# Kernel tuning notes

Hardware: AMD Instinct MI355X
Metric: run time of the kernel (lower is better)

Reference implementation:

```python
import jax, jax.numpy as jnp
import numpy as np

B, MQ, MK = 8, 512, 2048
Q_DIM, KV_DIM = 1024, 256
H = 8
QKC, VC = 1024, 1024
DQ, DV = QKC // H, VC // H
EPS = 1e-5  # nn.LayerNorm default


def _layer_norm(x, w, b):
    m = jnp.mean(x, axis=-1, keepdims=True)
    v = jnp.var(x, axis=-1, keepdims=True)
    return (x - m) * jax.lax.rsqrt(v + EPS) * w + b


def setup_inputs() -> dict:
    key = jax.random.key(0)
    ks = jax.random.split(key, 12)
    hidden_states = jax.random.normal(ks[0], (B, MQ, Q_DIM), dtype=jnp.float32)
    inputs = jax.random.normal(ks[1], (B, MK, KV_DIM), dtype=jnp.float32)
    # ragged per-batch kv lengths -> prefix-valid mask (matches keys[i, :n] packing)
    lengths = jax.random.randint(ks[2], (B,), MK // 4, MK + 1)
    inputs_mask = (jnp.arange(MK)[None, :] < lengths[:, None]).astype(jnp.int32)
    s = 0.02
    return {
        "hidden_states": hidden_states,
        "inputs": inputs,
        "inputs_mask": inputs_mask,
        "ln1_w": jnp.ones((Q_DIM,), jnp.float32),
        "ln1_b": jnp.zeros((Q_DIM,), jnp.float32),
        "ln2_w": jnp.ones((KV_DIM,), jnp.float32),
        "ln2_b": jnp.zeros((KV_DIM,), jnp.float32),
        "Wq": s * jax.random.normal(ks[3], (Q_DIM, QKC), dtype=jnp.float32),
        "bq": jnp.zeros((QKC,), jnp.float32),
        "Wk": s * jax.random.normal(ks[4], (KV_DIM, QKC), dtype=jnp.float32),
        "bk": jnp.zeros((QKC,), jnp.float32),
        "Wv": s * jax.random.normal(ks[5], (KV_DIM, VC), dtype=jnp.float32),
        "bv": jnp.zeros((VC,), jnp.float32),
    }


def reference(hidden_states, inputs, inputs_mask, ln1_w, ln1_b, ln2_w, ln2_b,
              Wq, bq, Wk, bk, Wv, bv):
    hs = _layer_norm(hidden_states, ln1_w, ln1_b)      # [B, MQ, Q_DIM]
    kv = _layer_norm(inputs, ln2_w, ln2_b)             # [B, MK, KV_DIM]

    q = (hs @ Wq + bq).reshape(B, MQ, H, DQ)           # [B, MQ, H, DQ]
    k = (kv @ Wk + bk).reshape(B, MK, H, DQ)           # [B, MK, H, DQ]
    v = (kv @ Wv + bv).reshape(B, MK, H, DV)           # [B, MK, H, DV]

    scores = jnp.einsum("bqhd,bkhd->bhqk", q, k) / jnp.sqrt(jnp.float32(DQ))
    mask_f = inputs_mask.astype(scores.dtype)          # [B, MK]
    neg = jnp.finfo(scores.dtype).min
    scores = scores + (1.0 - mask_f)[:, None, None, :] * neg
    probs = jax.nn.softmax(scores, axis=-1)            # [B, H, MQ, MK]

    ctx = jnp.einsum("bhqk,bkhd->bqhd", probs, v)      # [B, MQ, H, DV]
    return ctx.reshape(B, MQ, H * DV)
```

## Files before the change

### kernel.cpp

```cpp
#include <hip/hip_runtime.h>

#define DI __device__ __forceinline__

typedef _Float16 f16x8 __attribute__((ext_vector_type(8)));
typedef _Float16 f16x4 __attribute__((ext_vector_type(4)));
typedef float    f32x4 __attribute__((ext_vector_type(4)));

namespace {

constexpr int kB  = 8;
constexpr int kMQ = 512;
constexpr int kMK = 2048;
constexpr int kQKC = 1024;
constexpr int kVC  = 1024;

DI void gload16(const void* g, void* l) {
  __builtin_amdgcn_global_load_lds(
      (const __attribute__((address_space(1))) void*)g,
      (__attribute__((address_space(3))) void*)l, 16, 0, 0);
}

DI f32x4 mfma16(f16x8 a, f16x8 b, f32x4 c) {
  return __builtin_amdgcn_mfma_f32_16x16x32_f16(a, b, c, 0, 0, 0);
}

DI f32x4 mfma16k16(f16x4 a, f16x4 b, f32x4 c) {
  return __builtin_amdgcn_mfma_f32_16x16x16f16(a, b, c, 0, 0, 0);
}

template<int K, int N>
DI void transpose_dev(const float* __restrict__ W, _Float16* __restrict__ WT,
                      int bid, float (*t)[65]) {
  int nt = bid % (N / 64), kt = bid / (N / 64);
  int k0 = kt * 64, n0 = nt * 64;
  int tid = threadIdx.x;
#pragma unroll
  for (int j = 0; j < 16; ++j) {
    int e = tid + j * 256;
    int r = e >> 6, c = e & 63;
    t[r][c] = W[(size_t)(k0 + r) * N + n0 + c];
  }
  __syncthreads();
#pragma unroll
  for (int j = 0; j < 16; ++j) {
    int e = tid + j * 256;
    int r = e >> 6, c = e & 63;
    WT[(size_t)(n0 + r) * K + k0 + c] = (_Float16)t[c][r];
  }
}

DI void ln1024_dev(const float* __restrict__ x, const float* __restrict__ w,
                   const float* __restrict__ bb, _Float16* __restrict__ y,
                   int row, float* red) {
  int tid = threadIdx.x;
  const float4* xr = (const float4*)(x + (size_t)row * 1024);
  float4 v = xr[tid];
  float s = v.x + v.y + v.z + v.w;
  float q = v.x * v.x + v.y * v.y + v.z * v.z + v.w * v.w;
#pragma unroll
  for (int m = 32; m; m >>= 1) { s += __shfl_xor(s, m); q += __shfl_xor(q, m); }
  if ((tid & 63) == 0) { red[tid >> 6] = s; red[4 + (tid >> 6)] = q; }
  __syncthreads();
  s = red[0] + red[1] + red[2] + red[3];
  q = red[4] + red[5] + red[6] + red[7];
  float mean = s * (1.0f / 1024.0f);
  float var = q * (1.0f / 1024.0f) - mean * mean;
  float inv = rsqrtf(var + 1e-5f);
  f16x4 o;
  const float* wp = w + tid * 4;
  const float* bp = bb + tid * 4;
  o[0] = (_Float16)((v.x - mean) * inv * wp[0] + bp[0]);
  o[1] = (_Float16)((v.y - mean) * inv * wp[1] + bp[1]);
  o[2] = (_Float16)((v.z - mean) * inv * wp[2] + bp[2]);
  o[3] = (_Float16)((v.w - mean) * inv * wp[3] + bp[3]);
  *(f16x4*)(y + (size_t)row * 1024 + tid * 4) = o;
}

DI void ln256_dev(const float* __restrict__ x, const float* __restrict__ w,
                  const float* __restrict__ bb, _Float16* __restrict__ y, int bid) {
  int tid = threadIdx.x;
  int lane = tid & 63, wv = tid >> 6;
  size_t row = (size_t)bid * 4 + wv;
  const float4* xr = (const float4*)(x + row * 256);
  float4 v = xr[lane];
  float s = v.x + v.y + v.z + v.w;
  float q = v.x * v.x + v.y * v.y + v.z * v.z + v.w * v.w;
#pragma unroll
  for (int m = 32; m; m >>= 1) { s += __shfl_xor(s, m); q += __shfl_xor(q, m); }
  float mean = s * (1.0f / 256.0f);
  float var = q * (1.0f / 256.0f) - mean * mean;
  float inv = rsqrtf(var + 1e-5f);
  f16x4 o;
  const float* wp = w + lane * 4;
  const float* bp = bb + lane * 4;
  o[0] = (_Float16)((v.x - mean) * inv * wp[0] + bp[0]);
  o[1] = (_Float16)((v.y - mean) * inv * wp[1] + bp[1]);
  o[2] = (_Float16)((v.z - mean) * inv * wp[2] + bp[2]);
  o[3] = (_Float16)((v.w - mean) * inv * wp[3] + bp[3]);
  *(f16x4*)(y + row * 256 + lane * 4) = o;
}

__global__ __launch_bounds__(256) void prep_all(
    const float* __restrict__ Wq, const float* __restrict__ Wk, const float* __restrict__ Wv,
    _Float16* __restrict__ WqT, _Float16* __restrict__ WkT, _Float16* __restrict__ WvT,
    const float* __restrict__ hs, const float* __restrict__ ln1w, const float* __restrict__ ln1b,
    _Float16* __restrict__ hsln,
    const float* __restrict__ xin, const float* __restrict__ ln2w, const float* __restrict__ ln2b,
    _Float16* __restrict__ kvln) {
  __shared__ float tbuf[64][65];
  int bid = blockIdx.x;
  if (bid < 256) {
    transpose_dev<1024, 1024>(Wq, WqT, bid, tbuf);
  } else if (bid < 320) {
    transpose_dev<256, 1024>(Wk, WkT, bid - 256, tbuf);
  } else if (bid < 384) {
    transpose_dev<256, 1024>(Wv, WvT, bid - 320, tbuf);
  } else if (bid < 4480) {
    ln1024_dev(hs, ln1w, ln1b, hsln, bid - 384, (float*)tbuf);
  } else {
    ln256_dev(xin, ln2w, ln2b, kvln, bid - 4480);
  }
}

template<int M, int N, int K, bool BIAS_ROW, int MMODE, bool CM>
DI void gemm_dev(const _Float16* __restrict__ A, const _Float16* __restrict__ Bt,
                 const float* __restrict__ bias, const int* __restrict__ msk,
                 _Float16* __restrict__ C, int bid,
                 _Float16 (*As)[128 * 64], _Float16 (*Bs)[128 * 64]) {
  int tid = threadIdx.x, lane = tid & 63;
  int w = tid >> 6, wr = w >> 1, wc = w & 1;
  constexpr int NT = N / 128;
  constexpr int MT = M / 128;
  constexpr int KT = K / 64;
  int mt, nt;
  if constexpr (CM) { mt = bid % MT; nt = bid / MT; }
  else              { mt = bid / NT; nt = bid % NT; }
  if constexpr (MMODE == 1) { if (msk[mt * 128] == 0) return; }
  if constexpr (MMODE == 2) { if (msk[nt * 128] == 0) return; }
  const int l15 = lane & 15, l4 = lane >> 4;

  f32x4 acc[4][4] = {};

  const int rS = tid >> 3;
  const int cpS = tid & 7;

  auto stage = [&](int kt, int bufi) {
#pragma unroll
    for (int j = 0; j < 4; ++j) {
      int rr = rS + j * 32;
      int cg = cpS ^ (rr & 7);
      gload16(A  + ((size_t)(mt * 128 + rr) * K + kt * 64 + cg * 8),
              (char*)As[bufi] + j * 4096 + tid * 16);
      gload16(Bt + ((size_t)(nt * 128 + rr) * K + kt * 64 + cg * 8),
              (char*)Bs[bufi] + j * 4096 + tid * 16);
    }
  };

  stage(0, 0);
  __syncthreads();

  for (int kt = 0; kt < KT; ++kt) {
    int cur = kt & 1;
    if (kt + 1 < KT) stage(kt + 1, cur ^ 1);
#pragma unroll
    for (int ss = 0; ss < 2; ++ss) {
      f16x8 a[4], b[4];
#pragma unroll
      for (int m = 0; m < 4; ++m) {
        int ra = wr * 64 + m * 16 + l15;
        int cl = ss * 4 + l4;
        a[m] = *(const f16x8*)((const char*)As[cur] + ra * 128 + ((cl ^ (ra & 7)) << 4));
        int rb = wc * 64 + m * 16 + l15;
        b[m] = *(const f16x8*)((const char*)Bs[cur] + rb * 128 + ((cl ^ (rb & 7)) << 4));
      }
#pragma unroll
      for (int m = 0; m < 4; ++m)
#pragma unroll
        for (int n = 0; n < 4; ++n)
          acc[m][n] = mfma16(a[m], b[n], acc[m][n]);
    }
    __syncthreads();
  }

#pragma unroll
  for (int m = 0; m < 4; ++m) {
#pragma unroll
    for (int n = 0; n < 4; ++n) {
      int gi0 = mt * 128 + wr * 64 + m * 16 + l4 * 4;
      int gj  = nt * 128 + wc * 64 + n * 16 + l15;
#pragma unroll
      for (int r = 0; r < 4; ++r) {
        int gi = gi0 + r;
        float v = acc[m][n][r] + (BIAS_ROW ? bias[gi] : bias[gj]);
        C[(size_t)gi * N + gj] = (_Float16)v;
      }
    }
  }
}

__global__ __launch_bounds__(256) void gemm_all(
    const _Float16* __restrict__ hsln, const _Float16* __restrict__ WqT,
    const float* __restrict__ bq, _Float16* __restrict__ qbf,
    const _Float16* __restrict__ kvln, const _Float16* __restrict__ WkT,
    const float* __restrict__ bk, _Float16* __restrict__ kbf,
    const _Float16* __restrict__ WvT, const float* __restrict__ bv,
    _Float16* __restrict__ vT, const int* __restrict__ msk) {
  __shared__ _Float16 As[2][128 * 64];
  __shared__ _Float16 Bs[2][128 * 64];
  int bid = blockIdx.x;
  if (bid < 256) {
    gemm_dev<4096, 1024, 1024, false, 0, true>(hsln, WqT, bq, nullptr, qbf, bid, As, Bs);
  } else if (bid < 1280) {
    gemm_dev<16384, 1024, 256, false, 1, true>(kvln, WkT, bk, msk, kbf, bid - 256, As, Bs);
  } else {
    gemm_dev<1024, 16384, 256, true, 2, false>(WvT, kvln, bv, msk, vT, bid - 1280, As, Bs);
  }
}

__global__ __launch_bounds__(512, 2) void attn_kernel(const _Float16* __restrict__ qm,
                                                      const _Float16* __restrict__ km,
                                                      const _Float16* __restrict__ vT,
                                                      const int* __restrict__ msk,
                                                      float* __restrict__ out) {
  __shared__ __align__(16) char smem[132096];
  _Float16* Ksp = (_Float16*)smem;
  _Float16* Vsp = (_Float16*)(smem + 65536);
  float*    mlb = (float*)(smem + 131072);

  int tid = threadIdx.x, lane = tid & 63, w = tid >> 6;
  int bh = blockIdx.x & 63, qt = blockIdx.x >> 6;
  int h = bh & 7, b = bh >> 3;
  const int l15 = lane & 15, l4 = lane >> 4;
  const int wq = w & 3;
  const int g  = w >> 2;

  int vld = (lane < 32) ? msk[b * kMK + lane * 64] : 0;
  int nt64 = __popcll(__ballot(vld != 0));
  int lv = msk[b * kMK + (nt64 - 1) * 64 + lane];
  int L = (nt64 - 1) * 64 + __popcll(__ballot(lv != 0));
  int ntiles = (L + 127) >> 7;

  f16x8 qf[2][4];
#pragma unroll
  for (int m = 0; m < 2; ++m)
#pragma unroll
    for (int kc = 0; kc < 4; ++kc)
      qf[m][kc] = *(const f16x8*)(qm +
          (size_t)(b * kMQ + qt * 128 + wq * 32 + m * 16 + l15) * kQKC +
          h * 128 + kc * 32 + l4 * 8);

  f32x4 o[2][8] = {};
  float rm[2] = {-1e30f, -1e30f}, rl[2] = {0.0f, 0.0f};

  const float sl2 = 0.08838834764831845f * 1.4426950408889634f;

  const int rKV = tid >> 4, cp = tid & 15;

  auto stage = [&](int kt, int bufi) {
#pragma unroll
    for (int j = 0; j < 4; ++j) {
      int rr = rKV + j * 32;
      int cg = cp ^ (rr & 7);
      gload16(km + (size_t)(b * kMK + kt * 128 + rr) * kQKC + h * 128 + cg * 8,
              (char*)Ksp + bufi * 32768 + j * 8192 + tid * 16);
    }
#pragma unroll
    for (int j = 0; j < 4; ++j) {
      int dv = rKV + j * 32;
      int cg = cp ^ (dv & 15);
      gload16(vT + (size_t)(h * 128 + dv) * (kB * kMK) + (size_t)b * kMK + kt * 128 + cg * 8,
              (char*)Vsp + bufi * 32768 + j * 8192 + tid * 16);
    }
  };

  stage(0, 0);
  __syncthreads();

  for (int kt = 0; kt < ntiles; ++kt) {
    int cur = kt & 1;
    if (kt + 1 < ntiles) stage(kt + 1, cur ^ 1);

    f32x4 sc[2][4] = {};
    __builtin_amdgcn_s_setprio(1);
#pragma unroll
    for (int kc = 0; kc < 4; ++kc) {
      f16x8 kb[4];
#pragma unroll
      for (int kf = 0; kf < 4; ++kf) {
        int rr = g * 64 + kf * 16 + l15;
        int cl = kc * 4 + l4;
        kb[kf] = *(const f16x8*)((const char*)Ksp + cur * 32768 + rr * 256 +
                                 ((cl ^ (rr & 7)) << 4));
      }
#pragma unroll
      for (int m = 0; m < 2; ++m)
#pragma unroll
        for (int kf = 0; kf < 4; ++kf)
          sc[m][kf] = mfma16(kb[kf], qf[m][kc], sc[m][kf]);
    }
    __builtin_amdgcn_s_setprio(0);

    if (kt == ntiles - 1) {
      int base = kt * 128 + g * 64;
#pragma unroll
      for (int kf = 0; kf < 4; ++kf)
#pragma unroll
        for (int r = 0; r < 4; ++r)
          if (base + kf * 16 + l4 * 4 + r >= L) {
            sc[0][kf][r] = -3e38f;
            sc[1][kf][r] = -3e38f;
          }
    }

    float mx[2];
#pragma unroll
    for (int m = 0; m < 2; ++m) {
      float v = sc[m][0][0];
#pragma unroll
      for (int kf = 0; kf < 4; ++kf)
#pragma unroll
        for (int r = 0; r < 4; ++r) v = fmaxf(v, sc[m][kf][r]);
      v = fmaxf(v, __shfl_xor(v, 16));
      v = fmaxf(v, __shfl_xor(v, 32));
      mx[m] = v;
    }
    float al[2] = {1.0f, 1.0f};
    if (__any(mx[0] > rm[0] || mx[1] > rm[1])) {
#pragma unroll
      for (int m = 0; m < 2; ++m) {
        float nm = fmaxf(rm[m], mx[m]);
        al[m] = __builtin_amdgcn_exp2f((rm[m] - nm) * sl2);
        rm[m] = nm;
#pragma unroll
        for (int n = 0; n < 8; ++n)
#pragma unroll
          for (int r = 0; r < 4; ++r) o[m][n][r] *= al[m];
      }
    }
    f16x4 pb[2][4];
#pragma unroll
    for (int m = 0; m < 2; ++m) {
      float nms = rm[m] * sl2;
      float ts = 0.0f;
#pragma unroll
      for (int kf = 0; kf < 4; ++kf)
#pragma unroll
        for (int r = 0; r < 4; ++r) {
          float p = __builtin_amdgcn_exp2f(sc[m][kf][r] * sl2 - nms);
          pb[m][kf][r] = (_Float16)p;
          ts += p;
        }
      ts += __shfl_xor(ts, 16);
      ts += __shfl_xor(ts, 32);
      rl[m] = rl[m] * al[m] + ts;
    }

    __builtin_amdgcn_s_setprio(1);
#pragma unroll
    for (int n = 0; n < 8; ++n) {
      int dv = n * 16 + l15;
#pragma unroll
      for (int kf = 0; kf < 4; ++kf) {
        int phys = (g * 8 + kf * 2 + (l4 >> 1)) ^ (dv & 15);
        f16x4 vb = *(const f16x4*)((const char*)Vsp + cur * 32768 +
                                   dv * 256 + (phys << 4) + (l4 & 1) * 8);
#pragma unroll
        for (int m = 0; m < 2; ++m)
          o[m][n] = mfma16k16(vb, pb[m][kf], o[m][n]);
      }
    }
    __builtin_amdgcn_s_setprio(0);
    __syncthreads();
  }

  float* Mbuf = (float*)smem;
  if (g == 1) {
#pragma unroll
    for (int m = 0; m < 2; ++m) {
#pragma unroll
      for (int n = 0; n < 8; ++n)
#pragma unroll
        for (int r = 0; r < 4; ++r)
          Mbuf[(n * 16 + l4 * 4 + r) * 128 + wq * 32 + m * 16 + l15] = o[m][n][r];
      if (l4 == 0) {
        mlb[(wq * 32 + m * 16 + l15) * 2 + 0] = rm[m];
        mlb[(wq * 32 + m * 16 + l15) * 2 + 1] = rl[m];
      }
    }
  }
  __syncthreads();
  if (g == 1) return;

#pragma unroll
  for (int m = 0; m < 2; ++m) {
    int ql = wq * 32 + m * 16 + l15;
    float m1 = mlb[ql * 2 + 0];
    float l1 = mlb[ql * 2 + 1];
    float mm = fmaxf(rm[m], m1);
    float w0 = __builtin_amdgcn_exp2f((rm[m] - mm) * sl2);
    float w1 = __builtin_amdgcn_exp2f((m1 - mm) * sl2);
    float inv = 1.0f / (rl[m] * w0 + l1 * w1);
    w0 *= inv; w1 *= inv;
    int qg = qt * 128 + ql;
#pragma unroll
    for (int n = 0; n < 8; ++n) {
      f32x4 ov;
#pragma unroll
      for (int r = 0; r < 4; ++r) {
        float o1 = Mbuf[(n * 16 + l4 * 4 + r) * 128 + ql];
        ov[r] = o[m][n][r] * w0 + o1 * w1;
      }
      *(f32x4*)(out + ((size_t)b * kMQ + qg) * kVC + h * 128 + n * 16 + l4 * 4) = ov;
    }
  }
}

}

extern "C" void kernel_launch(void* const* d_in, const int* in_sizes, int n_in,
                              void* d_out, int out_size, void* d_ws, size_t ws_size,
                              hipStream_t stream) {
  (void)in_sizes; (void)n_in; (void)out_size; (void)ws_size;
  const float* hs   = (const float*)d_in[0];
  const float* xin  = (const float*)d_in[1];
  const int*   msk  = (const int*)d_in[2];
  const float* ln1w = (const float*)d_in[3];
  const float* ln1b = (const float*)d_in[4];
  const float* ln2w = (const float*)d_in[5];
  const float* ln2b = (const float*)d_in[6];
  const float* Wq   = (const float*)d_in[7];
  const float* bq   = (const float*)d_in[8];
  const float* Wk   = (const float*)d_in[9];
  const float* bk   = (const float*)d_in[10];
  const float* Wv   = (const float*)d_in[11];
  const float* bv   = (const float*)d_in[12];
  float* out = (float*)d_out;

  char* ws = (char*)d_ws;
  _Float16* qbf  = (_Float16*)(ws + 0);
  _Float16* kbf  = (_Float16*)(ws + 8388608);
  _Float16* vT   = (_Float16*)(ws + 41943040);
  _Float16* hsln = (_Float16*)(ws + 75497472);
  _Float16* kvln = (_Float16*)(ws + 83886080);
  _Float16* WqT  = (_Float16*)(ws + 92274688);
  _Float16* WkT  = (_Float16*)(ws + 94371840);
  _Float16* WvT  = (_Float16*)(ws + 94896128);

  prep_all<<<8576, 256, 0, stream>>>(Wq, Wk, Wv, WqT, WkT, WvT,
                                     hs, ln1w, ln1b, hsln,
                                     xin, ln2w, ln2b, kvln);
  gemm_all<<<2304, 256, 0, stream>>>(hsln, WqT, bq, qbf,
                                     kvln, WkT, bk, kbf,
                                     WvT, bv, vT, msk);
  attn_kernel<<<256, 512, 0, stream>>>(qbf, kbf, vT, msk, out);
}
```

Baseline: 106.8 us.

## Split attention KV range across two blocks with sorted work list and combine kernel

Attention now runs 512 blocks, each covering half of the valid KV tiles for one (batch, head, query tile), so more CUs are occupied than with 256 blocks. A work list built in the prep kernel orders the items so batches with longer valid lengths are scheduled first, easing load imbalance. Partial outputs are stored as fp16 along with their max and sum, and a new combine kernel merges the two halves into the fp32 output. This adds a kernel launch, extra global traffic for the partials, and fp16 rounding of intermediate results. The hsln and WqT buffers are reused as scratch for the partials.

Result: slower. 116.4 us (+9.0%).

```diff
diff --git a/kernel.cpp b/kernel.cpp
--- a/kernel.cpp
+++ b/kernel.cpp
@@ -106,7 +106,8 @@
     const float* __restrict__ hs, const float* __restrict__ ln1w, const float* __restrict__ ln1b,
     _Float16* __restrict__ hsln,
     const float* __restrict__ xin, const float* __restrict__ ln2w, const float* __restrict__ ln2b,
-    _Float16* __restrict__ kvln) {
+    _Float16* __restrict__ kvln,
+    const int* __restrict__ msk, int* __restrict__ work) {
   __shared__ float tbuf[64][65];
   int bid = blockIdx.x;
   if (bid < 256) {
@@ -117,8 +118,39 @@
     transpose_dev<256, 1024>(Wv, WvT, bid - 320, tbuf);
   } else if (bid < 4480) {
     ln1024_dev(hs, ln1w, ln1b, hsln, bid - 384, (float*)tbuf);
+  } else if (bid < 8576) {
+    ln256_dev(xin, ln2w, ln2b, kvln, bid - 4480);
   } else {
-    ln256_dev(xin, ln2w, ln2b, kvln, bid - 4480);
+    int* wbuf = (int*)tbuf;
+    int t = threadIdx.x;
+    int b = t >> 5, tile = t & 31;
+    wbuf[t] = (msk[b * kMK + tile * 64] != 0) ? 1 : 0;
+    __syncthreads();
+    if (t < 8) {
+      int s = 0;
+      for (int i = 0; i < 32; ++i) s += wbuf[t * 32 + i];
+      wbuf[256 + t] = s;
+    }
+    __syncthreads();
+    if (t == 0) {
+      int ord[8];
+      for (int i = 0; i < 8; ++i) ord[i] = i;
+      for (int i = 1; i < 8; ++i) {
+        int o = ord[i], j = i;
+        while (j > 0 && wbuf[256 + ord[j - 1]] < wbuf[256 + o]) { ord[j] = ord[j - 1]; --j; }
+        ord[j] = o;
+      }
+      for (int i = 0; i < 8; ++i) wbuf[264 + i] = ord[i];
+    }
+    __syncthreads();
+#pragma unroll
+    for (int k = 0; k < 2; ++k) {
+      int p = t + k * 256;
+      int h = p & 7, idx = (p >> 3) & 7, s = p >> 6;
+      int qt = idx >> 1, half = idx & 1;
+      int bb2 = wbuf[264 + s];
+      work[p] = (bb2 * 8 + h) | (qt << 6) | (half << 8);
+    }
   }
 }
 
@@ -221,14 +253,17 @@
                                                       const _Float16* __restrict__ km,
                                                       const _Float16* __restrict__ vT,
                                                       const int* __restrict__ msk,
-                                                      float* __restrict__ out) {
+                                                      const int* __restrict__ work,
+                                                      _Float16* __restrict__ pO,
+                                                      float* __restrict__ pML) {
   __shared__ __align__(16) char smem[132096];
   _Float16* Ksp = (_Float16*)smem;
   _Float16* Vsp = (_Float16*)(smem + 65536);
   float*    mlb = (float*)(smem + 131072);
 
   int tid = threadIdx.x, lane = tid & 63, w = tid >> 6;
-  int bh = blockIdx.x & 63, qt = blockIdx.x >> 6;
+  int v = work[blockIdx.x];
+  int bh = v & 63, qt = (v >> 6) & 3, half = (v >> 8) & 1;
   int h = bh & 7, b = bh >> 3;
   const int l15 = lane & 15, l4 = lane >> 4;
   const int wq = w & 3;
@@ -239,6 +274,9 @@
   int lv = msk[b * kMK + (nt64 - 1) * 64 + lane];
   int L = (nt64 - 1) * 64 + __popcll(__ballot(lv != 0));
   int ntiles = (L + 127) >> 7;
+  int h1 = (ntiles + 1) >> 1;
+  int t0 = half ? h1 : 0;
+  int t1 = half ? ntiles : h1;
 
   f16x8 qf[2][4];
 #pragma unroll
@@ -273,12 +311,12 @@
     }
   };
 
-  stage(0, 0);
+  stage(t0, 0);
   __syncthreads();
 
-  for (int kt = 0; kt < ntiles; ++kt) {
-    int cur = kt & 1;
-    if (kt + 1 < ntiles) stage(kt + 1, cur ^ 1);
+  for (int kt = t0; kt < t1; ++kt) {
+    int cur = (kt - t0) & 1;
+    if (kt + 1 < t1) stage(kt + 1, cur ^ 1);
 
     f32x4 sc[2][4] = {};
     __builtin_amdgcn_s_setprio(1);
@@ -315,14 +353,14 @@
     float mx[2];
 #pragma unroll
     for (int m = 0; m < 2; ++m) {
-      float v = sc[m][0][0];
+      float vv = sc[m][0][0];
 #pragma unroll
       for (int kf = 0; kf < 4; ++kf)
 #pragma unroll
-        for (int r = 0; r < 4; ++r) v = fmaxf(v, sc[m][kf][r]);
-      v = fmaxf(v, __shfl_xor(v, 16));
-      v = fmaxf(v, __shfl_xor(v, 32));
-      mx[m] = v;
+        for (int r = 0; r < 4; ++r) vv = fmaxf(vv, sc[m][kf][r]);
+      vv = fmaxf(vv, __shfl_xor(vv, 16));
+      vv = fmaxf(vv, __shfl_xor(vv, 32));
+      mx[m] = vv;
     }
     float al[2] = {1.0f, 1.0f};
     if (__any(mx[0] > rm[0] || mx[1] > rm[1])) {
@@ -391,6 +429,8 @@
   __syncthreads();
   if (g == 1) return;
 
+  int item = bh * 8 + qt * 2 + half;
+  _Float16* po = pO + (size_t)item * 16384;
 #pragma unroll
   for (int m = 0; m < 2; ++m) {
     int ql = wq * 32 + m * 16 + l15;
@@ -399,19 +439,58 @@
     float mm = fmaxf(rm[m], m1);
     float w0 = __builtin_amdgcn_exp2f((rm[m] - mm) * sl2);
     float w1 = __builtin_amdgcn_exp2f((m1 - mm) * sl2);
-    float inv = 1.0f / (rl[m] * w0 + l1 * w1);
-    w0 *= inv; w1 *= inv;
-    int qg = qt * 128 + ql;
+    float lmerged = rl[m] * w0 + l1 * w1;
 #pragma unroll
     for (int n = 0; n < 8; ++n) {
-      f32x4 ov;
+      f16x4 st;
 #pragma unroll
       for (int r = 0; r < 4; ++r) {
         float o1 = Mbuf[(n * 16 + l4 * 4 + r) * 128 + ql];
-        ov[r] = o[m][n][r] * w0 + o1 * w1;
-      }
-      *(f32x4*)(out + ((size_t)b * kMQ + qg) * kVC + h * 128 + n * 16 + l4 * 4) = ov;
-    }
+        st[r] = (_Float16)(o[m][n][r] * w0 + o1 * w1);
+      }
+      *(f16x4*)(po + ql * 128 + n * 16 + l4 * 4) = st;
+    }
+    if (l4 == 0) {
+      pML[(item * 128 + ql) * 2 + 0] = mm;
+      pML[(item * 128 + ql) * 2 + 1] = lmerged;
+    }
+  }
+}
+
+__global__ __launch_bounds__(256) void combine_kernel(const _Float16* __restrict__ pO,
+                                                      const float* __restrict__ pML,
+                                                      float* __restrict__ out) {
+  int cid = blockIdx.x;
+  int bh = cid >> 2, qt = cid & 3;
+  int h = bh & 7, b = bh >> 3;
+  int t = threadIdx.x;
+  int q = t >> 1, c = t & 1;
+  const float sl2 = 0.08838834764831845f * 1.4426950408889634f;
+
+  int i1 = bh * 8 + qt * 2, i2 = i1 + 1;
+  float m1 = pML[(i1 * 128 + q) * 2 + 0], l1 = pML[(i1 * 128 + q) * 2 + 1];
+  float m2 = pML[(i2 * 128 + q) * 2 + 0], l2 = pML[(i2 * 128 + q) * 2 + 1];
+  float m = fmaxf(m1, m2);
+  float w1 = __builtin_amdgcn_exp2f((m1 - m) * sl2);
+  float w2 = __builtin_amdgcn_exp2f((m2 - m) * sl2);
+  float inv = 1.0f / (l1 * w1 + l2 * w2);
+  w1 *= inv; w2 *= inv;
+
+  const _Float16* p1 = pO + (size_t)i1 * 16384 + q * 128 + c * 64;
+  const _Float16* p2 = pO + (size_t)i2 * 16384 + q * 128 + c * 64;
+  float* orow = out + ((size_t)b * kMQ + qt * 128 + q) * kVC + h * 128 + c * 64;
+#pragma unroll
+  for (int j = 0; j < 8; ++j) {
+    f16x8 a = *(const f16x8*)(p1 + j * 8);
+    f16x8 bb = *(const f16x8*)(p2 + j * 8);
+    f32x4 o0, o1;
+#pragma unroll
+    for (int r = 0; r < 4; ++r) {
+      o0[r] = (float)a[r] * w1 + (float)bb[r] * w2;
+      o1[r] = (float)a[4 + r] * w1 + (float)bb[4 + r] * w2;
+    }
+    *(f32x4*)(orow + j * 8) = o0;
+    *(f32x4*)(orow + j * 8 + 4) = o1;
   }
 }
 
@@ -445,12 +524,17 @@
   _Float16* WqT  = (_Float16*)(ws + 92274688);
   _Float16* WkT  = (_Float16*)(ws + 94371840);
   _Float16* WvT  = (_Float16*)(ws + 94896128);
-
-  prep_all<<<8576, 256, 0, stream>>>(Wq, Wk, Wv, WqT, WkT, WvT,
+  int*      work = (int*)(ws + 95420416);
+  _Float16* pO   = hsln;
+  float*    pML  = (float*)WqT;
+
+  prep_all<<<8577, 256, 0, stream>>>(Wq, Wk, Wv, WqT, WkT, WvT,
                                      hs, ln1w, ln1b, hsln,
-                                     xin, ln2w, ln2b, kvln);
+                                     xin, ln2w, ln2b, kvln,
+                                     msk, work);
   gemm_all<<<2304, 256, 0, stream>>>(hsln, WqT, bq, qbf,
                                      kvln, WkT, bk, kbf,
                                      WvT, bv, vT, msk);
-  attn_kernel<<<256, 512, 0, stream>>>(qbf, kbf, vT, msk, out);
-}
+  attn_kernel<<<512, 512, 0, stream>>>(qbf, kbf, vT, msk, work, pO, pML);
+  combine_kernel<<<256, 256, 0, stream>>>(pO, pML, out);
+}
```

## Software-pipeline QK^T of next tile with softmax and PV of current tile

Applied to the files above, without the earlier changes.

Splits K and V staging into separate loads, with K prefetched two tiles ahead and V one tile ahead. The QK^T MFMAs for tile kt+1 are issued before the softmax and PV of tile kt, so matrix work can overlap with the exp/max/sum VALU work. The aim is to hide softmax latency and global-load latency behind MFMA issue. In exchange it holds an extra score accumulator in registers, which raises VGPR pressure and may lower occupancy.

Result: no change. 107.3 us (+0.5%).

```diff
diff --git a/kernel.cpp b/kernel.cpp
--- a/kernel.cpp
+++ b/kernel.cpp
@@ -250,13 +250,15 @@
           h * 128 + kc * 32 + l4 * 8);
 
   f32x4 o[2][8] = {};
+  f32x4 sp[2][4] = {};
+  f32x4 sn[2][4] = {};
   float rm[2] = {-1e30f, -1e30f}, rl[2] = {0.0f, 0.0f};
 
   const float sl2 = 0.08838834764831845f * 1.4426950408889634f;
 
   const int rKV = tid >> 4, cp = tid & 15;
 
-  auto stage = [&](int kt, int bufi) {
+  auto stage_k = [&](int kt, int bufi) {
 #pragma unroll
     for (int j = 0; j < 4; ++j) {
       int rr = rKV + j * 32;
@@ -264,6 +266,8 @@
       gload16(km + (size_t)(b * kMK + kt * 128 + rr) * kQKC + h * 128 + cg * 8,
               (char*)Ksp + bufi * 32768 + j * 8192 + tid * 16);
     }
+  };
+  auto stage_v = [&](int kt, int bufi) {
 #pragma unroll
     for (int j = 0; j < 4; ++j) {
       int dv = rKV + j * 32;
@@ -273,14 +277,7 @@
     }
   };
 
-  stage(0, 0);
-  __syncthreads();
-
-  for (int kt = 0; kt < ntiles; ++kt) {
-    int cur = kt & 1;
-    if (kt + 1 < ntiles) stage(kt + 1, cur ^ 1);
-
-    f32x4 sc[2][4] = {};
+  auto qk = [&](int bufi, f32x4 (&sc)[2][4]) {
     __builtin_amdgcn_s_setprio(1);
 #pragma unroll
     for (int kc = 0; kc < 4; ++kc) {
@@ -289,7 +286,7 @@
       for (int kf = 0; kf < 4; ++kf) {
         int rr = g * 64 + kf * 16 + l15;
         int cl = kc * 4 + l4;
-        kb[kf] = *(const f16x8*)((const char*)Ksp + cur * 32768 + rr * 256 +
+        kb[kf] = *(const f16x8*)((const char*)Ksp + bufi * 32768 + rr * 256 +
                                  ((cl ^ (rr & 7)) << 4));
       }
 #pragma unroll
@@ -299,6 +296,27 @@
           sc[m][kf] = mfma16(kb[kf], qf[m][kc], sc[m][kf]);
     }
     __builtin_amdgcn_s_setprio(0);
+  };
+
+  stage_k(0, 0);
+  stage_v(0, 0);
+  if (ntiles > 1) stage_k(1, 1);
+  __syncthreads();
+  qk(0, sp);
+
+  for (int kt = 0; kt < ntiles; ++kt) {
+    int cur = kt & 1;
+    if (kt + 2 < ntiles) stage_k(kt + 2, cur);
+    if (kt + 1 < ntiles) stage_v(kt + 1, cur ^ 1);
+
+    if (kt + 1 < ntiles) {
+#pragma unroll
+      for (int m = 0; m < 2; ++m)
+#pragma unroll
+        for (int kf = 0; kf < 4; ++kf)
+          sn[m][kf] = f32x4{0.0f, 0.0f, 0.0f, 0.0f};
+      qk(cur ^ 1, sn);
+    }
 
     if (kt == ntiles - 1) {
       int base = kt * 128 + g * 64;
@@ -307,22 +325,22 @@
 #pragma unroll
         for (int r = 0; r < 4; ++r)
           if (base + kf * 16 + l4 * 4 + r >= L) {
-            sc[0][kf][r] = -3e38f;
-            sc[1][kf][r] = -3e38f;
+            sp[0][kf][r] = -3e38f;
+            sp[1][kf][r] = -3e38f;
           }
     }
 
     float mx[2];
 #pragma unroll
     for (int m = 0; m < 2; ++m) {
-      float v = sc[m][0][0];
+      float vv = sp[m][0][0];
 #pragma unroll
       for (int kf = 0; kf < 4; ++kf)
 #pragma unroll
-        for (int r = 0; r < 4; ++r) v = fmaxf(v, sc[m][kf][r]);
-      v = fmaxf(v, __shfl_xor(v, 16));
-      v = fmaxf(v, __shfl_xor(v, 32));
-      mx[m] = v;
+        for (int r = 0; r < 4; ++r) vv = fmaxf(vv, sp[m][kf][r]);
+      vv = fmaxf(vv, __shfl_xor(vv, 16));
+      vv = fmaxf(vv, __shfl_xor(vv, 32));
+      mx[m] = vv;
     }
     float al[2] = {1.0f, 1.0f};
     if (__any(mx[0] > rm[0] || mx[1] > rm[1])) {
@@ -346,7 +364,7 @@
       for (int kf = 0; kf < 4; ++kf)
 #pragma unroll
         for (int r = 0; r < 4; ++r) {
-          float p = __builtin_amdgcn_exp2f(sc[m][kf][r] * sl2 - nms);
+          float p = __builtin_amdgcn_exp2f(sp[m][kf][r] * sl2 - nms);
           pb[m][kf][r] = (_Float16)p;
           ts += p;
         }
@@ -370,9 +388,18 @@
       }
     }
     __builtin_amdgcn_s_setprio(0);
-    __syncthreads();
-  }
-
+
+    if (kt + 1 < ntiles) {
+      __syncthreads();
+#pragma unroll
+      for (int m = 0; m < 2; ++m)
+#pragma unroll
+        for (int kf = 0; kf < 4; ++kf)
+          sp[m][kf] = sn[m][kf];
+    }
+  }
+
+  __syncthreads();
   float* Mbuf = (float*)smem;
   if (g == 1) {
 #pragma unroll
```
